# Performance work log

Hardware: AMD Instinct MI355X
Metric: run time of the kernel (lower is better)

Reference implementation:

```python
import jax, jax.numpy as jnp
import numpy as np

# Production-scale graph dims (see shape_source)
N = 50000      # nodes
E = 800000     # edges (avg degree 16)
C_IN = 128     # input feature dim
H = 96         # hidden (per species: prey X and predator Y)
C_OUT = 40     # num_classes
L = 5          # LVConv layers
DT = 0.05      # integration step


def setup_inputs() -> dict:
    key = jax.random.key(0)
    ks = jax.random.split(key, 14)
    x = jax.random.normal(ks[0], (N, C_IN), jnp.float32)
    edge_index = jax.random.randint(ks[1], (2, E), 0, N, dtype=jnp.int32)
    # lift linears
    Wx = jax.random.normal(ks[2], (C_IN, H), jnp.float32) / np.sqrt(C_IN)
    bx = jnp.zeros((H,), jnp.float32)
    Wy = jax.random.normal(ks[3], (C_IN, H), jnp.float32) / np.sqrt(C_IN)
    by = jnp.zeros((H,), jnp.float32)
    # per-layer Lotka-Volterra coefficients (per-channel), small positive scale
    alpha = 0.1 * jax.random.uniform(ks[4], (L, H), jnp.float32)
    beta  = 0.1 * jax.random.uniform(ks[5], (L, H), jnp.float32)
    gamma = 0.1 * jax.random.uniform(ks[6], (L, H), jnp.float32)
    delta = 0.1 * jax.random.uniform(ks[7], (L, H), jnp.float32)
    # readout on concat([X, Y])
    Wr = jax.random.normal(ks[8], (2 * H, C_OUT), jnp.float32) / np.sqrt(2 * H)
    br = jnp.zeros((C_OUT,), jnp.float32)
    return {"x": x, "edge_index": edge_index, "Wx": Wx, "bx": bx,
            "Wy": Wy, "by": by, "alpha": alpha, "beta": beta,
            "gamma": gamma, "delta": delta, "Wr": Wr, "br": br}


def reference(x, edge_index, Wx, bx, Wy, by, alpha, beta, gamma, delta, Wr, br):
    src, dst = edge_index[0], edge_index[1]
    # in-degree for mean aggregation over incoming edges
    deg = jax.ops.segment_sum(jnp.ones((E,), x.dtype), dst, num_segments=N)
    deg_inv = (1.0 / jnp.maximum(deg, 1.0))[:, None]  # [N,1]

    def mean_agg(v):  # [N,H] -> [N,H] neighbor mean (src -> dst)
        return jax.ops.segment_sum(v[src], dst, num_segments=N) * deg_inv

    # lift to prey (X) and predator (Y) populations
    X = jnp.tanh(x @ Wx + bx)
    Y = jnp.tanh(x @ Wy + by)
    # dropout is identity in eval mode (training=False)
    for l in range(L):
        aggX = mean_agg(X)
        aggY = mean_agg(Y)
        # explicit-Euler Lotka-Volterra dynamics on the graph
        Xn = X + DT * X * (alpha[l] - beta[l] * aggY)
        Yn = Y + DT * Y * (-gamma[l] + delta[l] * aggX)
        X, Y = Xn, Yn
    h = jnp.concatenate([X, Y], axis=-1)  # [N, 2H]
    return h @ Wr + br
```

## Files before the change

kernel.cpp:

```cpp
#include <hip/hip_runtime.h>
#include <hip/hip_bf16.h>
#include <hip/hip_fp16.h>


#define HDIM 96
#define CIN 128
#define COUT 40
#define NLAYER 5
#define DTC 0.05f

#define BK_SHIFT 7
#define BK_SIZE 128
#define EPB 2048
#define BCAP 3072
#define BSTRIDE 4096

typedef float  vfloat2 __attribute__((ext_vector_type(2)));
typedef float  vfloat4 __attribute__((ext_vector_type(4)));
typedef short  vshort8 __attribute__((ext_vector_type(8)));

__device__ __forceinline__ unsigned bf16_rne(float f) {
    unsigned u = __float_as_uint(f);
    return (u + 0x7fffu + ((u >> 16) & 1u)) >> 16;
}

__device__ __forceinline__ unsigned pack_bf16_pair(float xf, float yf) {
    return bf16_rne(xf) | (bf16_rne(yf) << 16);
}

__device__ __forceinline__ unsigned pack_f16_pair(float a, float b) {
    unsigned ha = (unsigned)__half_as_ushort(__float2half_rn(a));
    unsigned hb = (unsigned)__half_as_ushort(__float2half_rn(b));
    return ha | (hb << 16);
}

__device__ __forceinline__ float f16_lo(unsigned u) {
    return __half2float(__ushort_as_half((unsigned short)(u & 0xffffu)));
}
__device__ __forceinline__ float f16_hi(unsigned u) {
    return __half2float(__ushort_as_half((unsigned short)(u >> 16)));
}

__device__ __forceinline__ unsigned pack_fp8_quad(float x0, float y0, float x1, float y1) {
    int lo = __builtin_amdgcn_cvt_pk_fp8_f32(x0, y0, 0, false);
    int full = __builtin_amdgcn_cvt_pk_fp8_f32(x1, y1, lo, true);
    return (unsigned)full;
}

__device__ __forceinline__ float fast_tanh(float x) {
    float e = __expf(2.0f * x);
    return 1.0f - 2.0f * __builtin_amdgcn_rcpf(e + 1.0f);
}


__global__ __launch_bounds__(256) void wprep_kernel(
    const float* __restrict__ Wx, const float* __restrict__ bx,
    const float* __restrict__ Wy, const float* __restrict__ by,
    unsigned short* __restrict__ WcT, float* __restrict__ bc,
    int* __restrict__ gcur, int NB,
    unsigned* __restrict__ F0, unsigned* __restrict__ F1, int N) {
    int t = blockIdx.x * blockDim.x + threadIdx.x;
    if (t < NB) gcur[t] = 0;
    if (t < 192 * 128) {
        int cc = t >> 7;
        int k = t & 127;
        int h = cc >> 1;
        float w = (cc & 1) ? Wy[k * HDIM + h] : Wx[k * HDIM + h];
        WcT[cc * 128 + k] = (unsigned short)bf16_rne(w);
    }
    if (t < 192) {
        int h = t >> 1;
        bc[t] = (t & 1) ? by[h] : bx[h];
    }
    if (blockIdx.x == 0 && threadIdx.x < 48) {
        int plane = threadIdx.x >> 4, d = threadIdx.x & 15;
        size_t o = ((size_t)plane * (N + 1) + N) * 16 + d;
        F0[o] = 0u;
        F1[o] = 0u;
    }
}


__global__ __launch_bounds__(256) void bscatter_kernel(
    const int* __restrict__ src, const int* __restrict__ dst,
    int* __restrict__ gcur, unsigned* __restrict__ packed, int E, int NB) {
    __shared__ int h[512];
    __shared__ int cur[512];
    for (int i = threadIdx.x; i < NB; i += 256) h[i] = 0;
    __syncthreads();
    int base = blockIdx.x * EPB;
    int end = min(E, base + EPB);
    for (int e = base + threadIdx.x; e < end; e += 256)
        atomicAdd(&h[dst[e] >> BK_SHIFT], 1);
    __syncthreads();
    for (int i = threadIdx.x; i < NB; i += 256)
        cur[i] = h[i] ? atomicAdd(&gcur[i], h[i]) : 0;
    __syncthreads();
    for (int e = base + threadIdx.x; e < end; e += 256) {
        int d = dst[e];
        int b = d >> BK_SHIFT;
        int pos = atomicAdd(&cur[b], 1);
        if (pos < BCAP)
            packed[(size_t)b * BCAP + pos] =
                (unsigned)src[e] | ((unsigned)(d & (BK_SIZE - 1)) << 17);
    }
}


__global__ __launch_bounds__(256) void bcsr_kernel(
    const unsigned* __restrict__ packed, const int* __restrict__ gcur,
    uint2* __restrict__ rowinfo, unsigned short* __restrict__ csr, int N, int NB) {
    __shared__ int ldeg[BK_SIZE];
    __shared__ int sscan[BK_SIZE];
    __shared__ int lcur[BK_SIZE];
    int b = blockIdx.x;
    int t = threadIdx.x;
    int cnt = min(gcur[b], BCAP);
    const unsigned* pk = packed + (size_t)b * BCAP;
    int wbase = b * BSTRIDE;
    if (t < BK_SIZE) ldeg[t] = 0;
    __syncthreads();
    for (int e = t; e < cnt; e += 256)
        atomicAdd(&ldeg[(pk[e] >> 17) & (BK_SIZE - 1)], 1);
    __syncthreads();
    int deg = 0, pad = 0;
    if (t < BK_SIZE) {
        deg = ldeg[t];
        pad = (deg + 7) & ~7;
        sscan[t] = pad;
    }
    __syncthreads();
    for (int off = 1; off < BK_SIZE; off <<= 1) {
        int tv = (t < BK_SIZE && t >= off) ? sscan[t - off] : 0;
        __syncthreads();
        if (t < BK_SIZE) sscan[t] += tv;
        __syncthreads();
    }
    int gpos = 0;
    if (t < BK_SIZE) {
        gpos = wbase + sscan[t] - pad;
        lcur[t] = gpos;
        int node = b * BK_SIZE + t;
        if (node < N) {
            rowinfo[node] = make_uint2(
                (unsigned)gpos | ((unsigned)(pad >> 2) << 21),
                __float_as_uint(1.0f / fmaxf((float)deg, 1.0f)));
        }
    }
    __syncthreads();
    for (int e = t; e < cnt; e += 256) {
        unsigned p = pk[e];
        int l = (p >> 17) & (BK_SIZE - 1);
        int pos = atomicAdd(&lcur[l], 1);
        csr[pos] = (unsigned short)(p & 0x1FFFFu);
    }
    __syncthreads();
    if (t < BK_SIZE) {
        for (int p = lcur[t]; p < gpos + pad; p++) csr[p] = (unsigned short)N;
    }
}


#define LW_STRIDE 136
#define TILE_STRIDE 200

__global__ __launch_bounds__(256) void lift_mfma_kernel(
    const float* __restrict__ x, const unsigned short* __restrict__ WcT,
    const float* __restrict__ bc, unsigned* __restrict__ S,
    unsigned* __restrict__ F, int N) {
    __shared__ __align__(16) char smem[192 * LW_STRIDE * 2];
    __shared__ float sBc[192];
    unsigned short* sW = (unsigned short*)smem;
    unsigned short* tile = (unsigned short*)smem;
    int t = threadIdx.x;

    {
        const unsigned* g = (const unsigned*)WcT;
        unsigned* s = (unsigned*)sW;
        for (int i = t; i < 192 * 64; i += 256) {
            int cc = i >> 6;
            int kp = i & 63;
            s[cc * (LW_STRIDE / 2) + kp] = g[i];
        }
    }
    if (t < 192) sBc[t] = bc[t];
    __syncthreads();

    int wv = t >> 6;
    int lane = t & 63;
    int quad = lane >> 4;
    int m = lane & 15;
    int mbase = blockIdx.x * 64 + wv * 16;

    int anode = mbase + m;
    if (anode >= N) anode = N - 1;
    const float* xrow = x + (size_t)anode * CIN;

    vfloat4 acc[12];
#pragma unroll
    for (int i = 0; i < 12; i++) acc[i] = (vfloat4){0.f, 0.f, 0.f, 0.f};

#pragma unroll
    for (int kt = 0; kt < 4; kt++) {
        int k0 = kt * 32 + quad * 8;
        float4 xa = *(const float4*)(xrow + k0);
        float4 xb = *(const float4*)(xrow + k0 + 4);
        uint4 ua;
        ua.x = pack_bf16_pair(xa.x, xa.y);
        ua.y = pack_bf16_pair(xa.z, xa.w);
        ua.z = pack_bf16_pair(xb.x, xb.y);
        ua.w = pack_bf16_pair(xb.z, xb.w);
        vshort8 a = *(vshort8*)&ua;
#pragma unroll
        for (int nt = 0; nt < 12; nt++) {
            vshort8 b = *(const vshort8*)&sW[(nt * 16 + m) * LW_STRIDE + k0];
            acc[nt] = __builtin_amdgcn_mfma_f32_16x16x32_bf16(a, b, acc[nt], 0, 0, 0);
        }
    }

    __syncthreads();
#pragma unroll
    for (int nt = 0; nt < 12; nt++) {
        int ccb = nt * 16 + m;
        float bco = sBc[ccb];
#pragma unroll
        for (int r = 0; r < 4; r++) {
            int nl = wv * 16 + quad * 4 + r;
            float v = fast_tanh(acc[nt][r] + bco);
            tile[nl * TILE_STRIDE + ccb] = __half_as_ushort(__float2half_rn(v));
        }
    }
    __syncthreads();

    int nbase = blockIdx.x * 64;
#pragma unroll
    for (int i = 0; i < 6; i++) {
        int idx = i * 256 + t;
        int nl = idx / 24;
        int pos = idx - nl * 24;
        int node = nbase + nl;
        uint4 u = *(const uint4*)&tile[nl * TILE_STRIDE + pos * 8];
        if (node < N) {
            *(uint4*)(S + (size_t)node * 96 + pos * 4) = u;
            float f0 = f16_lo(u.x), f1 = f16_hi(u.x);
            float f2 = f16_lo(u.y), f3 = f16_hi(u.y);
            float f4 = f16_lo(u.z), f5 = f16_hi(u.z);
            float f6 = f16_lo(u.w), f7 = f16_hi(u.w);
            uint2 fq = make_uint2(pack_fp8_quad(f0, f1, f2, f3),
                                  pack_fp8_quad(f4, f5, f6, f7));
            int plane = pos >> 3;
            int slot = (2 * pos) & 15;
            *(uint2*)(F + ((size_t)plane * (N + 1) + node) * 16 + slot) = fq;
        }
    }
}


#define SPAN_CAP 4096

__global__ __launch_bounds__(256) void layer_kernel(
    const unsigned* __restrict__ F, unsigned* __restrict__ S,
    unsigned* __restrict__ Fn,
    const uint2* __restrict__ rowinfo, const unsigned short* __restrict__ csr,
    const float* __restrict__ alpha, const float* __restrict__ beta,
    const float* __restrict__ gamma, const float* __restrict__ delta,
    int N, int nblk) {
    __shared__ __align__(16) unsigned short sidx[SPAN_CAP];
    int bid = blockIdx.x;
    int plane = bid / nblk;
    int tile = bid - plane * nblk;
    unsigned pstride = (unsigned)(N + 1) * 16u;
    const unsigned* Fp = F + (size_t)plane * pstride;

    int t = threadIdx.x;
    int wave = t >> 6;
    int lane = t & 63;
    int li = lane & 7;
    unsigned tli = (unsigned)(2 * li);

    int n0 = tile * 32;
    int nlast = min(n0 + 31, N - 1);
    unsigned ri0x = rowinfo[n0].x;
    unsigned riLx = rowinfo[nlast].x;
    unsigned beg0 = ri0x & 0x1FFFFFu;
    unsigned endL = (riLx & 0x1FFFFFu) + ((riLx >> 21) << 2);
    int span = (int)(endL - beg0);
    bool use_lds = (span <= SPAN_CAP);
    if (use_lds) {
        const uint4* gs = (const uint4*)(csr + beg0);
        uint4* ld = (uint4*)sidx;
        for (int i = t; i < (span >> 3); i += 256) ld[i] = gs[i];
    }

    int node = n0 + wave * 8 + (lane >> 3);
    bool nvalid = node < N;
    int nclamp = nvalid ? node : N - 1;
    uint2 ri = rowinfo[nclamp];
    unsigned beg = ri.x & 0x1FFFFFu;
    int cnt = nvalid ? (int)((ri.x >> 21) << 2) : 0;
    float dinv = __uint_as_float(ri.y);

    __syncthreads();

    vfloat2 a0 = {0.f, 0.f}, a1 = {0.f, 0.f}, a2 = {0.f, 0.f}, a3 = {0.f, 0.f};

#define UNP(u)                                                              \
    do {                                                                    \
        a0 += __builtin_amdgcn_cvt_pk_f32_fp8((int)(u).x, false);           \
        a1 += __builtin_amdgcn_cvt_pk_f32_fp8((int)(u).x, true);            \
        a2 += __builtin_amdgcn_cvt_pk_f32_fp8((int)(u).y, false);           \
        a3 += __builtin_amdgcn_cvt_pk_f32_fp8((int)(u).y, true);            \
    } while (0)

#define GBODY(WEXPR)                                                        \
    _Pragma("unroll 2")                                                     \
    for (int j = 0; j < cnt; j += 8) {                                      \
        uint4 w = WEXPR;                                                    \
        unsigned o0 = ((w.x & 0xffffu) << 4) + tli;                         \
        unsigned o1 = ((w.x >> 16) << 4) + tli;                             \
        unsigned o2 = ((w.y & 0xffffu) << 4) + tli;                         \
        unsigned o3 = ((w.y >> 16) << 4) + tli;                             \
        unsigned o4 = ((w.z & 0xffffu) << 4) + tli;                         \
        unsigned o5 = ((w.z >> 16) << 4) + tli;                             \
        unsigned o6 = ((w.w & 0xffffu) << 4) + tli;                         \
        unsigned o7 = ((w.w >> 16) << 4) + tli;                             \
        uint2 u0 = *(const uint2*)(Fp + o0);                                \
        uint2 u1 = *(const uint2*)(Fp + o1);                                \
        uint2 u2 = *(const uint2*)(Fp + o2);                                \
        uint2 u3 = *(const uint2*)(Fp + o3);                                \
        uint2 u4 = *(const uint2*)(Fp + o4);                                \
        uint2 u5 = *(const uint2*)(Fp + o5);                                \
        uint2 u6 = *(const uint2*)(Fp + o6);                                \
        uint2 u7 = *(const uint2*)(Fp + o7);                                \
        UNP(u0); UNP(u1); UNP(u2); UNP(u3);                                 \
        UNP(u4); UNP(u5); UNP(u6); UNP(u7);                                 \
    }

    if (use_lds) {
        unsigned lbeg = beg - beg0;
        GBODY((*(const uint4*)(sidx + lbeg + (unsigned)j)))
    } else {
        GBODY((*(const uint4*)(csr + beg + (unsigned)j)))
    }
#undef GBODY
#undef UNP

    if (!nvalid) return;

    int h0 = plane * 32 + 4 * li;
    float4 av = *(const float4*)(alpha + h0);
    float4 bv = *(const float4*)(beta + h0);
    float4 gv = *(const float4*)(gamma + h0);
    float4 dv = *(const float4*)(delta + h0);
    unsigned* srow = S + (size_t)node * 96 + h0;
    uint4 su = *(const uint4*)srow;

    float x0 = f16_lo(su.x), y0 = f16_hi(su.x);
    float x1 = f16_lo(su.y), y1 = f16_hi(su.y);
    float x2 = f16_lo(su.z), y2 = f16_hi(su.z);
    float x3 = f16_lo(su.w), y3 = f16_hi(su.w);

    float ox0 = x0 + DTC * x0 * (av.x - bv.x * (a0.y * dinv));
    float oy0 = y0 + DTC * y0 * (-gv.x + dv.x * (a0.x * dinv));
    float ox1 = x1 + DTC * x1 * (av.y - bv.y * (a1.y * dinv));
    float oy1 = y1 + DTC * y1 * (-gv.y + dv.y * (a1.x * dinv));
    float ox2 = x2 + DTC * x2 * (av.z - bv.z * (a2.y * dinv));
    float oy2 = y2 + DTC * y2 * (-gv.z + dv.z * (a2.x * dinv));
    float ox3 = x3 + DTC * x3 * (av.w - bv.w * (a3.y * dinv));
    float oy3 = y3 + DTC * y3 * (-gv.w + dv.w * (a3.x * dinv));

    uint4 so;
    so.x = pack_f16_pair(ox0, oy0);
    so.y = pack_f16_pair(ox1, oy1);
    so.z = pack_f16_pair(ox2, oy2);
    so.w = pack_f16_pair(ox3, oy3);
    *(uint4*)srow = so;

    if (Fn) {
        uint2 fo;
        fo.x = pack_fp8_quad(ox0, oy0, ox1, oy1);
        fo.y = pack_fp8_quad(ox2, oy2, ox3, oy3);
        *(uint2*)(Fn + (size_t)plane * pstride + (unsigned)node * 16u + tli) = fo;
    }
}


#define WG_STRIDE 200

__global__ __launch_bounds__(256) void readout_mfma_kernel(
    const unsigned short* __restrict__ sh, const float* __restrict__ Wr,
    const float* __restrict__ br, float* __restrict__ out, int N) {
    __shared__ unsigned short sW[48 * WG_STRIDE];
    __shared__ float sB[48];
    int t = threadIdx.x;

    for (int i = t; i < 48 * 192; i += 256) {
        int n = i / 192;
        int kk = i - n * 192;
        int h = kk >> 1;
        float w = 0.f;
        if (n < COUT) w = (kk & 1) ? Wr[(HDIM + h) * COUT + n] : Wr[h * COUT + n];
        sW[n * WG_STRIDE + kk] = __half_as_ushort(__float2half_rn(w));
    }
    if (t < 48) sB[t] = (t < COUT) ? br[t] : 0.f;
    __syncthreads();

    int wv = t >> 6;
    int lane = t & 63;
    int quad = lane >> 4;
    int m = lane & 15;
    int mbase = blockIdx.x * 64 + wv * 16;

    int anode = mbase + m;
    if (anode >= N) anode = N - 1;
    const unsigned short* arow = sh + (size_t)anode * 192;

    vfloat4 acc0 = {0.f, 0.f, 0.f, 0.f};
    vfloat4 acc1 = {0.f, 0.f, 0.f, 0.f};
    vfloat4 acc2 = {0.f, 0.f, 0.f, 0.f};

#pragma unroll
    for (int kt = 0; kt < 6; kt++) {
        int k0 = kt * 32 + quad * 8;
        vshort8 a = *(const vshort8*)(arow + k0);
        vshort8 b0 = *(const vshort8*)&sW[(0 * 16 + m) * WG_STRIDE + k0];
        vshort8 b1 = *(const vshort8*)&sW[(1 * 16 + m) * WG_STRIDE + k0];
        vshort8 b2 = *(const vshort8*)&sW[(2 * 16 + m) * WG_STRIDE + k0];
        acc0 = __builtin_amdgcn_mfma_f32_16x16x32_f16(a, b0, acc0, 0, 0, 0);
        acc1 = __builtin_amdgcn_mfma_f32_16x16x32_f16(a, b1, acc1, 0, 0, 0);
        acc2 = __builtin_amdgcn_mfma_f32_16x16x32_f16(a, b2, acc2, 0, 0, 0);
    }

    float bo0 = sB[m];
    float bo1 = sB[16 + m];
    float bo2 = (m < 8) ? sB[32 + m] : 0.f;
#pragma unroll
    for (int r = 0; r < 4; r++) {
        int node = mbase + quad * 4 + r;
        if (node < N) {
            float* orow = out + (size_t)node * COUT;
            orow[m] = acc0[r] + bo0;
            orow[16 + m] = acc1[r] + bo1;
            if (m < 8) orow[32 + m] = acc2[r] + bo2;
        }
    }
}


extern "C" void kernel_launch(void* const* d_in, const int* in_sizes, int n_in,
                              void* d_out, int out_size, void* d_ws, size_t ws_size,
                              hipStream_t stream) {
    const float* x     = (const float*)d_in[0];
    const int*   ei    = (const int*)d_in[1];
    const float* Wx    = (const float*)d_in[2];
    const float* bx    = (const float*)d_in[3];
    const float* Wy    = (const float*)d_in[4];
    const float* by    = (const float*)d_in[5];
    const float* alpha = (const float*)d_in[6];
    const float* beta  = (const float*)d_in[7];
    const float* gamma = (const float*)d_in[8];
    const float* delta = (const float*)d_in[9];
    const float* Wr    = (const float*)d_in[10];
    const float* br    = (const float*)d_in[11];

    const int N = in_sizes[0] / CIN;
    const int E = in_sizes[1] / 2;
    const int NB = (N + BK_SIZE - 1) >> BK_SHIFT;
    const int nchunk = (E + EPB - 1) / EPB;
    const int nblk = (N + 31) / 32;

    char* ws = (char*)d_ws;
    size_t off = 0;
    auto alloc = [&](size_t bytes) -> void* {
        off = (off + 255) & ~(size_t)255;
        void* p = ws + off;
        off += bytes;
        return p;
    };
    int* gcur          = (int*)alloc((size_t)NB * sizeof(int));
    unsigned* pckd     = (unsigned*)alloc((size_t)NB * BCAP * sizeof(unsigned));
    uint2* rowinfo     = (uint2*)alloc((size_t)N * sizeof(uint2));
    unsigned short* csr = (unsigned short*)alloc(((size_t)NB * BSTRIDE + 64) * sizeof(unsigned short));
    unsigned* Sa   = (unsigned*)alloc((size_t)N * 96 * sizeof(unsigned));
    unsigned* Fa   = (unsigned*)alloc((size_t)(N + 1) * 48 * sizeof(unsigned));
    unsigned* Fb   = (unsigned*)alloc((size_t)(N + 1) * 48 * sizeof(unsigned));
    unsigned short* WcT = (unsigned short*)alloc((size_t)192 * 128 * sizeof(unsigned short));
    float* bc      = (float*)alloc((size_t)192 * sizeof(float));
    (void)ws_size;

    const int* e_src = ei;
    const int* e_dst = ei + E;

    wprep_kernel<<<(192 * 128 + 255) / 256, 256, 0, stream>>>(
        Wx, bx, Wy, by, WcT, bc, gcur, NB, Fa, Fb, N);

    bscatter_kernel<<<nchunk, 256, 0, stream>>>(e_src, e_dst, gcur, pckd, E, NB);
    bcsr_kernel<<<NB, 256, 0, stream>>>(pckd, gcur, rowinfo, csr, N, NB);

    lift_mfma_kernel<<<(N + 63) / 64, 256, 0, stream>>>(x, WcT, bc, Sa, Fa, N);

    const unsigned* Fc = Fa;
    unsigned* Fnx = Fb;
    for (int l = 0; l < NLAYER; l++) {
        bool last = (l == NLAYER - 1);
        layer_kernel<<<3 * nblk, 256, 0, stream>>>(
            Fc, Sa, last ? (unsigned*)nullptr : Fnx,
            rowinfo, csr,
            alpha + l * HDIM, beta + l * HDIM, gamma + l * HDIM, delta + l * HDIM,
            N, nblk);
        const unsigned* tf = Fc; Fc = Fnx; Fnx = (unsigned*)tf;
    }

    readout_mfma_kernel<<<(N + 63) / 64, 256, 0, stream>>>(
        (const unsigned short*)Sa, Wr, br, (float*)d_out, N);
}
```

Before: 291.6 us.

## Process all three feature planes per block to reuse CSR index loads

The layer kernel no longer launches one block per (plane, 32-node tile). Each block now handles 64 nodes across all three fp8 feature planes, with each thread group looping over two node rows. The CSR neighbor indices are read from LDS once and reused for the gathers from all three planes, removing the triplicated index staging and address computation and raising memory-level parallelism per thread. In exchange the grid is a third the size, each thread holds more accumulator registers, and the LDS index buffer doubles, which may reduce occupancy.

```diff
diff --git a/kernel.cpp b/kernel.cpp
--- a/kernel.cpp
+++ b/kernel.cpp
@@ -256,7 +256,7 @@
 }
 
 
-#define SPAN_CAP 4096
+#define SPAN_CAP 8192
 
 __global__ __launch_bounds__(256) void layer_kernel(
     const unsigned* __restrict__ F, unsigned* __restrict__ S,
@@ -264,22 +264,22 @@
     const uint2* __restrict__ rowinfo, const unsigned short* __restrict__ csr,
     const float* __restrict__ alpha, const float* __restrict__ beta,
     const float* __restrict__ gamma, const float* __restrict__ delta,
-    int N, int nblk) {
+    int N) {
     __shared__ __align__(16) unsigned short sidx[SPAN_CAP];
-    int bid = blockIdx.x;
-    int plane = bid / nblk;
-    int tile = bid - plane * nblk;
     unsigned pstride = (unsigned)(N + 1) * 16u;
-    const unsigned* Fp = F + (size_t)plane * pstride;
+    const unsigned* F0 = F;
+    const unsigned* F1 = F + pstride;
+    const unsigned* F2 = F + 2 * (size_t)pstride;
 
     int t = threadIdx.x;
     int wave = t >> 6;
     int lane = t & 63;
     int li = lane & 7;
+    int g = lane >> 3;
     unsigned tli = (unsigned)(2 * li);
 
-    int n0 = tile * 32;
-    int nlast = min(n0 + 31, N - 1);
+    int n0 = blockIdx.x * 64;
+    int nlast = min(n0 + 63, N - 1);
     unsigned ri0x = rowinfo[n0].x;
     unsigned riLx = rowinfo[nlast].x;
     unsigned beg0 = ri0x & 0x1FFFFFu;
@@ -291,97 +291,115 @@
         uint4* ld = (uint4*)sidx;
         for (int i = t; i < (span >> 3); i += 256) ld[i] = gs[i];
     }
-
-    int node = n0 + wave * 8 + (lane >> 3);
-    bool nvalid = node < N;
-    int nclamp = nvalid ? node : N - 1;
-    uint2 ri = rowinfo[nclamp];
-    unsigned beg = ri.x & 0x1FFFFFu;
-    int cnt = nvalid ? (int)((ri.x >> 21) << 2) : 0;
-    float dinv = __uint_as_float(ri.y);
-
-    __syncthreads();
-
-    vfloat2 a0 = {0.f, 0.f}, a1 = {0.f, 0.f}, a2 = {0.f, 0.f}, a3 = {0.f, 0.f};
-
-#define UNP(u)                                                              \
+    __syncthreads();
+
+#define UNP(u, A0, A1, A2, A3)                                              \
     do {                                                                    \
-        a0 += __builtin_amdgcn_cvt_pk_f32_fp8((int)(u).x, false);           \
-        a1 += __builtin_amdgcn_cvt_pk_f32_fp8((int)(u).x, true);            \
-        a2 += __builtin_amdgcn_cvt_pk_f32_fp8((int)(u).y, false);           \
-        a3 += __builtin_amdgcn_cvt_pk_f32_fp8((int)(u).y, true);            \
+        A0 += __builtin_amdgcn_cvt_pk_f32_fp8((int)(u).x, false);           \
+        A1 += __builtin_amdgcn_cvt_pk_f32_fp8((int)(u).x, true);            \
+        A2 += __builtin_amdgcn_cvt_pk_f32_fp8((int)(u).y, false);           \
+        A3 += __builtin_amdgcn_cvt_pk_f32_fp8((int)(u).y, true);            \
     } while (0)
 
-#define GBODY(WEXPR)                                                        \
-    _Pragma("unroll 2")                                                     \
-    for (int j = 0; j < cnt; j += 8) {                                      \
-        uint4 w = WEXPR;                                                    \
-        unsigned o0 = ((w.x & 0xffffu) << 4) + tli;                         \
-        unsigned o1 = ((w.x >> 16) << 4) + tli;                             \
-        unsigned o2 = ((w.y & 0xffffu) << 4) + tli;                         \
-        unsigned o3 = ((w.y >> 16) << 4) + tli;                             \
-        unsigned o4 = ((w.z & 0xffffu) << 4) + tli;                         \
-        unsigned o5 = ((w.z >> 16) << 4) + tli;                             \
-        unsigned o6 = ((w.w & 0xffffu) << 4) + tli;                         \
-        unsigned o7 = ((w.w >> 16) << 4) + tli;                             \
-        uint2 u0 = *(const uint2*)(Fp + o0);                                \
-        uint2 u1 = *(const uint2*)(Fp + o1);                                \
-        uint2 u2 = *(const uint2*)(Fp + o2);                                \
-        uint2 u3 = *(const uint2*)(Fp + o3);                                \
-        uint2 u4 = *(const uint2*)(Fp + o4);                                \
-        uint2 u5 = *(const uint2*)(Fp + o5);                                \
-        uint2 u6 = *(const uint2*)(Fp + o6);                                \
-        uint2 u7 = *(const uint2*)(Fp + o7);                                \
-        UNP(u0); UNP(u1); UNP(u2); UNP(u3);                                 \
-        UNP(u4); UNP(u5); UNP(u6); UNP(u7);                                 \
-    }
-
-    if (use_lds) {
-        unsigned lbeg = beg - beg0;
-        GBODY((*(const uint4*)(sidx + lbeg + (unsigned)j)))
-    } else {
-        GBODY((*(const uint4*)(csr + beg + (unsigned)j)))
-    }
-#undef GBODY
+#define GATHER4(i0, i1, i2, i3)                                             \
+    do {                                                                    \
+        unsigned o0 = ((i0) << 4) + tli;                                    \
+        unsigned o1 = ((i1) << 4) + tli;                                    \
+        unsigned o2 = ((i2) << 4) + tli;                                    \
+        unsigned o3 = ((i3) << 4) + tli;                                    \
+        uint2 p00 = *(const uint2*)(F0 + o0);                               \
+        uint2 p01 = *(const uint2*)(F0 + o1);                               \
+        uint2 p02 = *(const uint2*)(F0 + o2);                               \
+        uint2 p03 = *(const uint2*)(F0 + o3);                               \
+        uint2 p10 = *(const uint2*)(F1 + o0);                               \
+        uint2 p11 = *(const uint2*)(F1 + o1);                               \
+        uint2 p12 = *(const uint2*)(F1 + o2);                               \
+        uint2 p13 = *(const uint2*)(F1 + o3);                               \
+        uint2 p20 = *(const uint2*)(F2 + o0);                               \
+        uint2 p21 = *(const uint2*)(F2 + o1);                               \
+        uint2 p22 = *(const uint2*)(F2 + o2);                               \
+        uint2 p23 = *(const uint2*)(F2 + o3);                               \
+        UNP(p00, a00, a01, a02, a03); UNP(p01, a00, a01, a02, a03);         \
+        UNP(p02, a00, a01, a02, a03); UNP(p03, a00, a01, a02, a03);         \
+        UNP(p10, a10, a11, a12, a13); UNP(p11, a10, a11, a12, a13);         \
+        UNP(p12, a10, a11, a12, a13); UNP(p13, a10, a11, a12, a13);         \
+        UNP(p20, a20, a21, a22, a23); UNP(p21, a20, a21, a22, a23);         \
+        UNP(p22, a20, a21, a22, a23); UNP(p23, a20, a21, a22, a23);         \
+    } while (0)
+
+#pragma unroll 1
+    for (int r = 0; r < 2; r++) {
+        int node = n0 + wave * 16 + r * 8 + g;
+        bool nvalid = node < N;
+        int nclamp = nvalid ? node : N - 1;
+        uint2 ri = rowinfo[nclamp];
+        unsigned beg = ri.x & 0x1FFFFFu;
+        int cnt = nvalid ? (int)((ri.x >> 21) << 2) : 0;
+        float dinv = __uint_as_float(ri.y);
+
+        vfloat2 a00 = {0.f, 0.f}, a01 = {0.f, 0.f}, a02 = {0.f, 0.f}, a03 = {0.f, 0.f};
+        vfloat2 a10 = {0.f, 0.f}, a11 = {0.f, 0.f}, a12 = {0.f, 0.f}, a13 = {0.f, 0.f};
+        vfloat2 a20 = {0.f, 0.f}, a21 = {0.f, 0.f}, a22 = {0.f, 0.f}, a23 = {0.f, 0.f};
+
+        if (use_lds) {
+            unsigned lbeg = beg - beg0;
+            for (int j = 0; j < cnt; j += 8) {
+                uint4 w = *(const uint4*)(sidx + lbeg + (unsigned)j);
+                GATHER4(w.x & 0xffffu, w.x >> 16, w.y & 0xffffu, w.y >> 16);
+                GATHER4(w.z & 0xffffu, w.z >> 16, w.w & 0xffffu, w.w >> 16);
+            }
+        } else {
+            for (int j = 0; j < cnt; j += 8) {
+                uint4 w = *(const uint4*)(csr + beg + (unsigned)j);
+                GATHER4(w.x & 0xffffu, w.x >> 16, w.y & 0xffffu, w.y >> 16);
+                GATHER4(w.z & 0xffffu, w.z >> 16, w.w & 0xffffu, w.w >> 16);
+            }
+        }
+
+        if (!nvalid) continue;
+
+#define UPD(P, A0, A1, A2, A3)                                              \
+    do {                                                                    \
+        int h0 = P * 32 + 4 * li;                                           \
+        float4 av = *(const float4*)(alpha + h0);                           \
+        float4 bv = *(const float4*)(beta + h0);                            \
+        float4 gv = *(const float4*)(gamma + h0);                           \
+        float4 dv = *(const float4*)(delta + h0);                           \
+        unsigned* srow = S + (size_t)node * 96 + h0;                        \
+        uint4 su = *(const uint4*)srow;                                     \
+        float x0 = f16_lo(su.x), y0 = f16_hi(su.x);                         \
+        float x1 = f16_lo(su.y), y1 = f16_hi(su.y);                         \
+        float x2 = f16_lo(su.z), y2 = f16_hi(su.z);                         \
+        float x3 = f16_lo(su.w), y3 = f16_hi(su.w);                         \
+        float ox0 = x0 + DTC * x0 * (av.x - bv.x * (A0.y * dinv));          \
+        float oy0 = y0 + DTC * y0 * (-gv.x + dv.x * (A0.x * dinv));         \
+        float ox1 = x1 + DTC * x1 * (av.y - bv.y * (A1.y * dinv));          \
+        float oy1 = y1 + DTC * y1 * (-gv.y + dv.y * (A1.x * dinv));         \
+        float ox2 = x2 + DTC * x2 * (av.z - bv.z * (A2.y * dinv));          \
+        float oy2 = y2 + DTC * y2 * (-gv.z + dv.z * (A2.x * dinv));         \
+        float ox3 = x3 + DTC * x3 * (av.w - bv.w * (A3.y * dinv));          \
+        float oy3 = y3 + DTC * y3 * (-gv.w + dv.w * (A3.x * dinv));         \
+        uint4 so;                                                           \
+        so.x = pack_f16_pair(ox0, oy0);                                     \
+        so.y = pack_f16_pair(ox1, oy1);                                     \
+        so.z = pack_f16_pair(ox2, oy2);                                     \
+        so.w = pack_f16_pair(ox3, oy3);                                     \
+        *(uint4*)srow = so;                                                 \
+        if (Fn) {                                                           \
+            uint2 fo;                                                       \
+            fo.x = pack_fp8_quad(ox0, oy0, ox1, oy1);                       \
+            fo.y = pack_fp8_quad(ox2, oy2, ox3, oy3);                       \
+            *(uint2*)(Fn + (size_t)P * pstride + (unsigned)node * 16u + tli) = fo; \
+        }                                                                   \
+    } while (0)
+
+        UPD(0, a00, a01, a02, a03);
+        UPD(1, a10, a11, a12, a13);
+        UPD(2, a20, a21, a22, a23);
+#undef UPD
+    }
+#undef GATHER4
 #undef UNP
-
-    if (!nvalid) return;
-
-    int h0 = plane * 32 + 4 * li;
-    float4 av = *(const float4*)(alpha + h0);
-    float4 bv = *(const float4*)(beta + h0);
-    float4 gv = *(const float4*)(gamma + h0);
-    float4 dv = *(const float4*)(delta + h0);
-    unsigned* srow = S + (size_t)node * 96 + h0;
-    uint4 su = *(const uint4*)srow;
-
-    float x0 = f16_lo(su.x), y0 = f16_hi(su.x);
-    float x1 = f16_lo(su.y), y1 = f16_hi(su.y);
-    float x2 = f16_lo(su.z), y2 = f16_hi(su.z);
-    float x3 = f16_lo(su.w), y3 = f16_hi(su.w);
-
-    float ox0 = x0 + DTC * x0 * (av.x - bv.x * (a0.y * dinv));
-    float oy0 = y0 + DTC * y0 * (-gv.x + dv.x * (a0.x * dinv));
-    float ox1 = x1 + DTC * x1 * (av.y - bv.y * (a1.y * dinv));
-    float oy1 = y1 + DTC * y1 * (-gv.y + dv.y * (a1.x * dinv));
-    float ox2 = x2 + DTC * x2 * (av.z - bv.z * (a2.y * dinv));
-    float oy2 = y2 + DTC * y2 * (-gv.z + dv.z * (a2.x * dinv));
-    float ox3 = x3 + DTC * x3 * (av.w - bv.w * (a3.y * dinv));
-    float oy3 = y3 + DTC * y3 * (-gv.w + dv.w * (a3.x * dinv));
-
-    uint4 so;
-    so.x = pack_f16_pair(ox0, oy0);
-    so.y = pack_f16_pair(ox1, oy1);
-    so.z = pack_f16_pair(ox2, oy2);
-    so.w = pack_f16_pair(ox3, oy3);
-    *(uint4*)srow = so;
-
-    if (Fn) {
-        uint2 fo;
-        fo.x = pack_fp8_quad(ox0, oy0, ox1, oy1);
-        fo.y = pack_fp8_quad(ox2, oy2, ox3, oy3);
-        *(uint2*)(Fn + (size_t)plane * pstride + (unsigned)node * 16u + tli) = fo;
-    }
 }
 
 
@@ -467,7 +485,7 @@
     const int E = in_sizes[1] / 2;
     const int NB = (N + BK_SIZE - 1) >> BK_SHIFT;
     const int nchunk = (E + EPB - 1) / EPB;
-    const int nblk = (N + 31) / 32;
+    const int nblk64 = (N + 63) / 64;
 
     char* ws = (char*)d_ws;
     size_t off = 0;
@@ -503,11 +521,11 @@
     unsigned* Fnx = Fb;
     for (int l = 0; l < NLAYER; l++) {
         bool last = (l == NLAYER - 1);
-        layer_kernel<<<3 * nblk, 256, 0, stream>>>(
+        layer_kernel<<<nblk64, 256, 0, stream>>>(
             Fc, Sa, last ? (unsigned*)nullptr : Fnx,
             rowinfo, csr,
             alpha + l * HDIM, beta + l * HDIM, gamma + l * HDIM, delta + l * HDIM,
-            N, nblk);
+            N);
         const unsigned* tf = Fc; Fc = Fnx; Fnx = (unsigned*)tf;
     }
 
```

Measured after the change: 355.7 us. +22.0%, slower.
